# Kernel optimization log

Hardware: AMD Instinct MI355X
Metric: run time of the kernel (lower is better)

Reference implementation:

```python
import jax, jax.numpy as jnp
import numpy as np

N = 50000
E = 800000
F_IN = 128
HID = 32
HEADS = 4
SLOPE = 0.2


def setup_inputs() -> dict:
    key = jax.random.key(0)
    ks = jax.random.split(key, 12)
    x = jax.random.normal(ks[0], (N, F_IN), dtype=jnp.float32)
    edge_index = jax.random.randint(ks[1], (2, E), 0, N, dtype=jnp.int64)
    edge_attr = jax.random.normal(ks[2], (E, 4), dtype=jnp.float32)
    s1 = 1.0 / np.sqrt(F_IN)
    s2 = 1.0 / np.sqrt(HID)
    W1 = jax.random.normal(ks[3], (F_IN, HEADS * HID), dtype=jnp.float32) * s1
    a_src1 = jax.random.normal(ks[4], (HEADS, HID), dtype=jnp.float32) * s2
    a_dst1 = jax.random.normal(ks[5], (HEADS, HID), dtype=jnp.float32) * s2
    b1 = jnp.zeros((HID,), dtype=jnp.float32)
    W2 = jax.random.normal(ks[6], (HID, 1), dtype=jnp.float32) * s2
    a_src2 = jax.random.normal(ks[7], (1, 1), dtype=jnp.float32)
    a_dst2 = jax.random.normal(ks[8], (1, 1), dtype=jnp.float32)
    b2 = jnp.zeros((1,), dtype=jnp.float32)
    return {"input_tensor": x, "edge_index": edge_index, "edge_attr": edge_attr,
            "W1": W1, "a_src1": a_src1, "a_dst1": a_dst1, "b1": b1,
            "W2": W2, "a_src2": a_src2, "a_dst2": a_dst2, "b2": b2}


def _gat_conv(x, src, dst, W, a_src, a_dst, b, heads, out_ch):
    n = x.shape[0]
    h = (x @ W).reshape(n, heads, out_ch)          # [N, H, C]
    alpha_src = jnp.sum(h * a_src, axis=-1)        # [N, H]
    alpha_dst = jnp.sum(h * a_dst, axis=-1)        # [N, H]
    e = alpha_src[src] + alpha_dst[dst]            # [E, H]
    e = jax.nn.leaky_relu(e, negative_slope=SLOPE)
    # segment softmax over edges grouped by destination node
    e_max = jax.ops.segment_max(e, dst, num_segments=n)
    e = jnp.exp(e - e_max[dst])
    denom = jax.ops.segment_sum(e, dst, num_segments=n)
    alpha = e / denom[dst]                         # [E, H]
    msg = h[src] * alpha[..., None]                # [E, H, C]
    out = jax.ops.segment_sum(msg, dst, num_segments=n)  # [N, H, C]
    return out.mean(axis=1) + b                    # concat=False -> mean over heads


def reference(input_tensor, edge_index, edge_attr, W1, a_src1, a_dst1, b1, W2, a_src2, a_dst2, b2):
    # PyG GATConv adds self-loops by default; edge_attr unused (edge_dim=None)
    loops = jnp.arange(N, dtype=edge_index.dtype)
    src = jnp.concatenate([edge_index[0], loops])
    dst = jnp.concatenate([edge_index[1], loops])
    x = _gat_conv(input_tensor, src, dst, W1, a_src1, a_dst1, b1, HEADS, HID)
    x = jax.nn.elu(x)
    x = _gat_conv(x, src, dst, W2, a_src2, a_dst2, b2, 1, 1)
    return x
```

## Files before the change

kernel.cpp:

```cpp
#include <hip/hip_runtime.h>
#include <hip/hip_fp16.h>
#include <math.h>
#include <stdint.h>

static constexpr int kN     = 50000;
static constexpr int kFIn   = 128;
static constexpr int kHeads = 4;
static constexpr int kScanB = 256;
static constexpr int kScanNB = (kN + kScanB - 1) / kScanB;

typedef _Float16 half8v  __attribute__((ext_vector_type(8)));
typedef float    floatx4 __attribute__((ext_vector_type(4)));

__device__ __forceinline__ float lrelu(float x) { return x > 0.f ? x : 0.2f * x; }

__device__ __forceinline__ float pack2h(float a, float b) {
    const __half2 h = __floats2half2_rn(a, b);
    return __uint_as_float(__builtin_bit_cast(uint32_t, h));
}

__global__ void k_init(int* __restrict__ p, int n) {
    int i = blockIdx.x * blockDim.x + threadIdx.x;
    if (i < n) p[i] = 0;
}

__global__ __launch_bounds__(256)
void k_gemm1(const float* __restrict__ x, const float* __restrict__ W1,
             __half* __restrict__ h1h, int nPass, int grid) {
    __shared__ __align__(16) float whf[128 * 16 * 4];
    __shared__ __align__(16) float xsf[32 * 16 * 4];
    const int t = threadIdx.x;
    const int l = t & 63;
    const int g = t >> 6;
    for (int idx = t; idx < 2048; idx += 256) {
        const int c = idx >> 7, col = idx & 127;
        float4 st;
        st.x = pack2h(W1[(8 * c + 0) * 128 + col], W1[(8 * c + 1) * 128 + col]);
        st.y = pack2h(W1[(8 * c + 2) * 128 + col], W1[(8 * c + 3) * 128 + col]);
        st.z = pack2h(W1[(8 * c + 4) * 128 + col], W1[(8 * c + 5) * 128 + col]);
        st.w = pack2h(W1[(8 * c + 6) * 128 + col], W1[(8 * c + 7) * 128 + col]);
        const int gran = col * 16 + ((c + col) & 15);
        *reinterpret_cast<float4*>(&whf[gran * 4]) = st;
    }
    __syncthreads();

    const int rt  = g & 1;
    const int ctB = (g >> 1) * 4;
    const int lm  = l & 15;
    const int lk  = l >> 4;

    for (int pass = blockIdx.x; pass < nPass; pass += grid) {
        const int nodeBase = pass * 32;
        for (int q = t; q < 512; q += 256) {
            const int nn = q >> 4, ck = q & 15;
            int n = nodeBase + nn; if (n >= kN) n = kN - 1;
            const float4 xa = *reinterpret_cast<const float4*>(&x[(size_t)n * 128 + ck * 8]);
            const float4 xb = *reinterpret_cast<const float4*>(&x[(size_t)n * 128 + ck * 8 + 4]);
            float4 st;
            st.x = pack2h(xa.x, xa.y);
            st.y = pack2h(xa.z, xa.w);
            st.z = pack2h(xb.x, xb.y);
            st.w = pack2h(xb.z, xb.w);
            const int gran = nn * 16 + ((ck + nn) & 15);
            *reinterpret_cast<float4*>(&xsf[gran * 4]) = st;
        }
        __syncthreads();

        floatx4 acc0 = {0.f, 0.f, 0.f, 0.f};
        floatx4 acc1 = {0.f, 0.f, 0.f, 0.f};
        floatx4 acc2 = {0.f, 0.f, 0.f, 0.f};
        floatx4 acc3 = {0.f, 0.f, 0.f, 0.f};
        const int node = rt * 16 + lm;
        const int ch0  = ctB * 16 + lm;
#pragma unroll
        for (int kk = 0; kk < 4; ++kk) {
            const int ck = lk + 4 * kk;
            const half8v af = *reinterpret_cast<const half8v*>(
                &xsf[(node * 16 + ((ck + node) & 15)) * 4]);
            const half8v b0 = *reinterpret_cast<const half8v*>(
                &whf[((ch0 +  0) * 16 + ((ck + ch0 +  0) & 15)) * 4]);
            const half8v b1 = *reinterpret_cast<const half8v*>(
                &whf[((ch0 + 16) * 16 + ((ck + ch0 + 16) & 15)) * 4]);
            const half8v b2 = *reinterpret_cast<const half8v*>(
                &whf[((ch0 + 32) * 16 + ((ck + ch0 + 32) & 15)) * 4]);
            const half8v b3 = *reinterpret_cast<const half8v*>(
                &whf[((ch0 + 48) * 16 + ((ck + ch0 + 48) & 15)) * 4]);
            acc0 = __builtin_amdgcn_mfma_f32_16x16x32_f16(af, b0, acc0, 0, 0, 0);
            acc1 = __builtin_amdgcn_mfma_f32_16x16x32_f16(af, b1, acc1, 0, 0, 0);
            acc2 = __builtin_amdgcn_mfma_f32_16x16x32_f16(af, b2, acc2, 0, 0, 0);
            acc3 = __builtin_amdgcn_mfma_f32_16x16x32_f16(af, b3, acc3, 0, 0, 0);
        }
        const int nrow0 = nodeBase + rt * 16 + lk * 4;
#pragma unroll
        for (int r = 0; r < 4; ++r) {
            const int n = nrow0 + r;
            if (n < kN) {
                h1h[(size_t)n * 128 + ch0     ] = __float2half(acc0[r]);
                h1h[(size_t)n * 128 + ch0 + 16] = __float2half(acc1[r]);
                h1h[(size_t)n * 128 + ch0 + 32] = __float2half(acc2[r]);
                h1h[(size_t)n * 128 + ch0 + 48] = __float2half(acc3[r]);
            }
        }
        __syncthreads();
    }
}

__global__ __launch_bounds__(256)
void k_logits(const __half* __restrict__ h1h,
              const float* __restrict__ a_src1, const float* __restrict__ a_dst1,
              float* __restrict__ asrc, float* __restrict__ adst) {
    const int n = blockIdx.x * 4 + (threadIdx.x >> 6);
    if (n >= kN) return;
    const int j = threadIdx.x & 63;
    const float2 f = __half22float2(*(const __half2*)&h1h[(size_t)n * 128 + 2 * j]);
    float ps = f.x * a_src1[2 * j] + f.y * a_src1[2 * j + 1];
    float pd = f.x * a_dst1[2 * j] + f.y * a_dst1[2 * j + 1];
#pragma unroll
    for (int off = 8; off >= 1; off >>= 1) {
        ps += __shfl_xor(ps, off, 64);
        pd += __shfl_xor(pd, off, 64);
    }
    if ((j & 15) == 0) {
        asrc[n * 4 + (j >> 4)] = ps;
        adst[n * 4 + (j >> 4)] = pd;
    }
}

__global__ void k_hist(const int* __restrict__ ei, int E, int* __restrict__ deg,
                       int* __restrict__ rank) {
    int i = blockIdx.x * blockDim.x + threadIdx.x;
    int total = E + kN;
    if (i >= total) return;
    int d = (i < E) ? ei[E + i] : (i - E);
    rank[i] = atomicAdd(&deg[d], 1);
}

__global__ void k_scan_a(const int* __restrict__ deg, int* __restrict__ loc, int* __restrict__ bsum) {
    __shared__ int tmp[kScanB];
    int t = threadIdx.x;
    int i = blockIdx.x * kScanB + t;
    int v = (i < kN) ? deg[i] : 0;
    tmp[t] = v;
    __syncthreads();
    for (int off = 1; off < kScanB; off <<= 1) {
        int add = (t >= off) ? tmp[t - off] : 0;
        __syncthreads();
        tmp[t] += add;
        __syncthreads();
    }
    if (i < kN) loc[i] = tmp[t] - v;
    if (t == kScanB - 1) bsum[blockIdx.x] = tmp[t];
}

__global__ void k_scan_b(int* __restrict__ bsum) {
    __shared__ int tmp[256];
    int t = threadIdx.x;
    int v = (t < kScanNB) ? bsum[t] : 0;
    tmp[t] = v;
    __syncthreads();
    for (int off = 1; off < 256; off <<= 1) {
        int add = (t >= off) ? tmp[t - off] : 0;
        __syncthreads();
        tmp[t] += add;
        __syncthreads();
    }
    if (t < kScanNB) bsum[t] = tmp[t] - v;
}

__global__ void k_scan_c(const int* __restrict__ loc, const int* __restrict__ bsum,
                         int* __restrict__ rowptr, int E2) {
    int i = blockIdx.x * kScanB + threadIdx.x;
    if (i < kN) rowptr[i] = loc[i] + bsum[blockIdx.x];
    if (i == 0) rowptr[kN] = E2;
}

__global__ void k_scatter(const int* __restrict__ ei, int E,
                          const int* __restrict__ rowptr, const int* __restrict__ rank,
                          int* __restrict__ es) {
    int i = blockIdx.x * blockDim.x + threadIdx.x;
    int total = E + kN;
    if (i >= total) return;
    int s, d;
    if (i < E) { s = ei[i]; d = ei[E + i]; } else { s = d = i - E; }
    es[rowptr[d] + rank[i]] = s;
}

__global__ __launch_bounds__(256)
void k_wgt(const int* __restrict__ rowptr, const int* __restrict__ es,
           const float* __restrict__ asrc, const float* __restrict__ adst,
           __half* __restrict__ alphaH) {
    const int n = blockIdx.x * 16 + (threadIdx.x >> 4);
    if (n >= kN) return;
    const int l = threadIdx.x & 15;
    const int beg = rowptr[n], end = rowptr[n + 1];
    const float ad0 = adst[n * 4 + 0], ad1 = adst[n * 4 + 1];
    const float ad2 = adst[n * 4 + 2], ad3 = adst[n * 4 + 3];
    float t0 = 0.f, t1 = 0.f, t2 = 0.f, t3 = 0.f;
    for (int p = beg + l; p < end; p += 16) {
        const int s = es[p];
        t0 += expf(lrelu(asrc[s * 4 + 0] + ad0));
        t1 += expf(lrelu(asrc[s * 4 + 1] + ad1));
        t2 += expf(lrelu(asrc[s * 4 + 2] + ad2));
        t3 += expf(lrelu(asrc[s * 4 + 3] + ad3));
    }
#pragma unroll
    for (int off = 8; off >= 1; off >>= 1) {
        t0 += __shfl_xor(t0, off, 64);
        t1 += __shfl_xor(t1, off, 64);
        t2 += __shfl_xor(t2, off, 64);
        t3 += __shfl_xor(t3, off, 64);
    }
    const float r0 = 1.f / t0, r1 = 1.f / t1, r2 = 1.f / t2, r3 = 1.f / t3;
    for (int p = beg + l; p < end; p += 16) {
        const int s = es[p];
        const float w0 = expf(lrelu(asrc[s * 4 + 0] + ad0)) * r0;
        const float w1 = expf(lrelu(asrc[s * 4 + 1] + ad1)) * r1;
        const float w2 = expf(lrelu(asrc[s * 4 + 2] + ad2)) * r2;
        const float w3 = expf(lrelu(asrc[s * 4 + 3] + ad3)) * r3;
        float2 st;
        st.x = pack2h(w0, w1);
        st.y = pack2h(w2, w3);
        *reinterpret_cast<float2*>(&alphaH[(size_t)p * 4]) = st;
    }
}

__global__ __launch_bounds__(256)
void k_agg1(const int* __restrict__ rowptr, const int* __restrict__ es,
            const __half* __restrict__ alphaH,
            const __half* __restrict__ h1h, const float* __restrict__ b1,
            const float* __restrict__ W2, float* __restrict__ h2) {
    const int n = blockIdx.x * 4 + (threadIdx.x >> 6);
    if (n >= kN) return;
    const int j  = threadIdx.x & 63;
    const int hh = j >> 4;
    const int beg = rowptr[n], end = rowptr[n + 1];
    const __half2* h12 = (const __half2*)h1h;
    __half2 accA = __floats2half2_rn(0.f, 0.f);
    __half2 accB = __floats2half2_rn(0.f, 0.f);
    int p = beg;
    for (; p + 4 <= end; p += 4) {
        const int s0 = es[p],     s1 = es[p + 1];
        const int s2 = es[p + 2], s3 = es[p + 3];
        const __half a0 = alphaH[(size_t)(p + 0) * 4 + hh];
        const __half a1 = alphaH[(size_t)(p + 1) * 4 + hh];
        const __half a2 = alphaH[(size_t)(p + 2) * 4 + hh];
        const __half a3 = alphaH[(size_t)(p + 3) * 4 + hh];
        const __half2 v0 = h12[(size_t)s0 * 64 + j];
        const __half2 v1 = h12[(size_t)s1 * 64 + j];
        const __half2 v2 = h12[(size_t)s2 * 64 + j];
        const __half2 v3 = h12[(size_t)s3 * 64 + j];
        accA = __hfma2(__half2half2(a0), v0, accA);
        accB = __hfma2(__half2half2(a1), v1, accB);
        accA = __hfma2(__half2half2(a2), v2, accA);
        accB = __hfma2(__half2half2(a3), v3, accB);
    }
    for (; p < end; ++p) {
        const int s0 = es[p];
        const __half a0 = alphaH[(size_t)p * 4 + hh];
        accA = __hfma2(__half2half2(a0), h12[(size_t)s0 * 64 + j], accA);
    }
    const float2 fa = __half22float2(accA);
    const float2 fb = __half22float2(accB);
    float vx = fa.x + fb.x;
    float vy = fa.y + fb.y;
    vx += __shfl_xor(vx, 32, 64); vy += __shfl_xor(vy, 32, 64);
    vx += __shfl_xor(vx, 16, 64); vy += __shfl_xor(vy, 16, 64);
    const int m = j & 15;
    float u0 = 0.25f * vx + b1[2 * m];
    float u1 = 0.25f * vy + b1[2 * m + 1];
    u0 = u0 > 0.f ? u0 : expf(u0) - 1.f;
    u1 = u1 > 0.f ? u1 : expf(u1) - 1.f;
    float tsum = u0 * W2[2 * m] + u1 * W2[2 * m + 1];
    tsum += __shfl_xor(tsum, 8, 64);
    tsum += __shfl_xor(tsum, 4, 64);
    tsum += __shfl_xor(tsum, 2, 64);
    tsum += __shfl_xor(tsum, 1, 64);
    if (j == 0) h2[n] = tsum;
}

__global__ __launch_bounds__(256)
void k_agg2(const int* __restrict__ rowptr, const int* __restrict__ es,
            const float* __restrict__ h2,
            const float* __restrict__ a_s2, const float* __restrict__ a_d2,
            const float* __restrict__ b2, float* __restrict__ out) {
    const int n = blockIdx.x * 16 + (threadIdx.x >> 4);
    if (n >= kN) return;
    const int l = threadIdx.x & 15;
    const float as = a_s2[0], ad = a_d2[0];
    const int beg = rowptr[n], end = rowptr[n + 1];
    const float hd = h2[n] * ad;
    float sw = 0.f, swh = 0.f;
    for (int p = beg + l; p < end; p += 16) {
        float hs = h2[es[p]];
        float w = expf(lrelu(hs * as + hd));
        sw += w;
        swh += w * hs;
    }
#pragma unroll
    for (int off = 8; off >= 1; off >>= 1) {
        sw  += __shfl_xor(sw, off, 64);
        swh += __shfl_xor(swh, off, 64);
    }
    if (l == 0) out[n] = swh / sw + b2[0];
}

extern "C" void kernel_launch(void* const* d_in, const int* in_sizes, int n_in,
                              void* d_out, int out_size, void* d_ws, size_t ws_size,
                              hipStream_t stream) {
    const float* x      = (const float*)d_in[0];
    const int*   ei     = (const int*)d_in[1];
    const float* W1     = (const float*)d_in[3];
    const float* a_src1 = (const float*)d_in[4];
    const float* a_dst1 = (const float*)d_in[5];
    const float* b1     = (const float*)d_in[6];
    const float* W2     = (const float*)d_in[7];
    const float* a_src2 = (const float*)d_in[8];
    const float* a_dst2 = (const float*)d_in[9];
    const float* b2     = (const float*)d_in[10];
    float* out = (float*)d_out;

    const int E  = in_sizes[1] / 2;
    const int E2 = E + kN;

    float*  ws    = (float*)d_ws;
    float*  asrc  = ws;
    float*  adst  = ws + 200000;
    float*  h2    = ws + 400000;
    __half* h1h   = (__half*)(ws + 450000);
    __half* alphaH= (__half*)(ws + 3650000);
    int*    ibase = (int*)(ws + 5350000);
    int*    es     = ibase;
    int*    deg    = ibase + 850000;
    int*    rank   = ibase + 900000;
    int*    loc    = ibase + 1750000;
    int*    rowptr = ibase + 1800000;
    int*    bsum   = ibase + 1850016;

    k_init<<<(kN + 255) / 256, 256, 0, stream>>>(deg, kN);

    k_hist<<<(E2 + 255) / 256, 256, 0, stream>>>(ei, E, deg, rank);
    k_scan_a<<<kScanNB, kScanB, 0, stream>>>(deg, loc, bsum);
    k_scan_b<<<1, 256, 0, stream>>>(bsum);
    k_scan_c<<<kScanNB, kScanB, 0, stream>>>(loc, bsum, rowptr, E2);

    {
        const int nPass = (kN + 31) / 32;
        const int grid  = 782;
        k_gemm1<<<grid, 256, 0, stream>>>(x, W1, h1h, nPass, grid);
    }

    k_logits<<<(kN + 3) / 4, 256, 0, stream>>>(h1h, a_src1, a_dst1, asrc, adst);

    k_scatter<<<(E2 + 255) / 256, 256, 0, stream>>>(ei, E, rowptr, rank, es);

    k_wgt<<<(kN + 15) / 16, 256, 0, stream>>>(rowptr, es, asrc, adst, alphaH);

    k_agg1<<<(kN + 3) / 4, 256, 0, stream>>>(rowptr, es, alphaH, h1h, b1, W2, h2);

    k_agg2<<<(kN + 15) / 16, 256, 0, stream>>>(rowptr, es, h2, a_src2, a_dst2, b2, out);
}
```

Measured before the change: 147.5 us.

## Split layer-1 aggregation per head into partial sums plus a finish kernel

Result: slower. 172.3 us (+16.9%).

```diff
diff --git a/kernel.cpp b/kernel.cpp
--- a/kernel.cpp
+++ b/kernel.cpp
@@ -225,49 +225,53 @@
 }
 
 __global__ __launch_bounds__(256)
-void k_agg1(const int* __restrict__ rowptr, const int* __restrict__ es,
-            const __half* __restrict__ alphaH,
-            const __half* __restrict__ h1h, const float* __restrict__ b1,
-            const float* __restrict__ W2, float* __restrict__ h2) {
-    const int n = blockIdx.x * 4 + (threadIdx.x >> 6);
-    if (n >= kN) return;
-    const int j  = threadIdx.x & 63;
-    const int hh = j >> 4;
+void k_agg1h(const int* __restrict__ rowptr, const int* __restrict__ es,
+             const __half* __restrict__ alphaH, const __half* __restrict__ h1h,
+             __half2* __restrict__ part) {
+    const int b    = blockIdx.x;
+    const int head = (b & 7) >> 1;
+    const int rank = (b >> 3) * 2 + (b & 1);
+    const int g    = threadIdx.x >> 6;
+    const int l    = threadIdx.x & 63;
+    const int sub  = l >> 4;
+    const int m    = l & 15;
+    const int n    = rank * 16 + g * 4 + sub;
+    if (n >= kN) return;
     const int beg = rowptr[n], end = rowptr[n + 1];
     const __half2* h12 = (const __half2*)h1h;
+    const int chOff = head * 16 + m;
     __half2 accA = __floats2half2_rn(0.f, 0.f);
     __half2 accB = __floats2half2_rn(0.f, 0.f);
     int p = beg;
-    for (; p + 4 <= end; p += 4) {
-        const int s0 = es[p],     s1 = es[p + 1];
-        const int s2 = es[p + 2], s3 = es[p + 3];
-        const __half a0 = alphaH[(size_t)(p + 0) * 4 + hh];
-        const __half a1 = alphaH[(size_t)(p + 1) * 4 + hh];
-        const __half a2 = alphaH[(size_t)(p + 2) * 4 + hh];
-        const __half a3 = alphaH[(size_t)(p + 3) * 4 + hh];
-        const __half2 v0 = h12[(size_t)s0 * 64 + j];
-        const __half2 v1 = h12[(size_t)s1 * 64 + j];
-        const __half2 v2 = h12[(size_t)s2 * 64 + j];
-        const __half2 v3 = h12[(size_t)s3 * 64 + j];
-        accA = __hfma2(__half2half2(a0), v0, accA);
-        accB = __hfma2(__half2half2(a1), v1, accB);
-        accA = __hfma2(__half2half2(a2), v2, accA);
-        accB = __hfma2(__half2half2(a3), v3, accB);
-    }
-    for (; p < end; ++p) {
+    for (; p + 2 <= end; p += 2) {
+        const int s0 = es[p], s1 = es[p + 1];
+        const __half a0 = alphaH[(size_t)p * 4 + head];
+        const __half a1 = alphaH[(size_t)(p + 1) * 4 + head];
+        accA = __hfma2(__half2half2(a0), h12[(size_t)s0 * 64 + chOff], accA);
+        accB = __hfma2(__half2half2(a1), h12[(size_t)s1 * 64 + chOff], accB);
+    }
+    if (p < end) {
         const int s0 = es[p];
-        const __half a0 = alphaH[(size_t)p * 4 + hh];
-        accA = __hfma2(__half2half2(a0), h12[(size_t)s0 * 64 + j], accA);
-    }
-    const float2 fa = __half22float2(accA);
-    const float2 fb = __half22float2(accB);
-    float vx = fa.x + fb.x;
-    float vy = fa.y + fb.y;
-    vx += __shfl_xor(vx, 32, 64); vy += __shfl_xor(vy, 32, 64);
-    vx += __shfl_xor(vx, 16, 64); vy += __shfl_xor(vy, 16, 64);
-    const int m = j & 15;
-    float u0 = 0.25f * vx + b1[2 * m];
-    float u1 = 0.25f * vy + b1[2 * m + 1];
+        const __half a0 = alphaH[(size_t)p * 4 + head];
+        accA = __hfma2(__half2half2(a0), h12[(size_t)s0 * 64 + chOff], accA);
+    }
+    part[((size_t)head * kN + n) * 16 + m] = __hadd2(accA, accB);
+}
+
+__global__ __launch_bounds__(256)
+void k_finish(const __half2* __restrict__ part, const float* __restrict__ b1,
+              const float* __restrict__ W2, float* __restrict__ h2) {
+    const int n = blockIdx.x * 16 + (threadIdx.x >> 4);
+    if (n >= kN) return;
+    const int m = threadIdx.x & 15;
+    float sx = 0.f, sy = 0.f;
+#pragma unroll
+    for (int h = 0; h < kHeads; ++h) {
+        const float2 v = __half22float2(part[((size_t)h * kN + n) * 16 + m]);
+        sx += v.x; sy += v.y;
+    }
+    float u0 = 0.25f * sx + b1[2 * m];
+    float u1 = 0.25f * sy + b1[2 * m + 1];
     u0 = u0 > 0.f ? u0 : expf(u0) - 1.f;
     u1 = u1 > 0.f ? u1 : expf(u1) - 1.f;
     float tsum = u0 * W2[2 * m] + u1 * W2[2 * m + 1];
@@ -275,7 +279,7 @@
     tsum += __shfl_xor(tsum, 4, 64);
     tsum += __shfl_xor(tsum, 2, 64);
     tsum += __shfl_xor(tsum, 1, 64);
-    if (j == 0) h2[n] = tsum;
+    if (m == 0) h2[n] = tsum;
 }
 
 __global__ __launch_bounds__(256)
@@ -322,19 +326,20 @@
     const int E  = in_sizes[1] / 2;
     const int E2 = E + kN;
 
-    float*  ws    = (float*)d_ws;
-    float*  asrc  = ws;
-    float*  adst  = ws + 200000;
-    float*  h2    = ws + 400000;
-    __half* h1h   = (__half*)(ws + 450000);
-    __half* alphaH= (__half*)(ws + 3650000);
-    int*    ibase = (int*)(ws + 5350000);
-    int*    es     = ibase;
-    int*    deg    = ibase + 850000;
-    int*    rank   = ibase + 900000;
-    int*    loc    = ibase + 1750000;
-    int*    rowptr = ibase + 1800000;
-    int*    bsum   = ibase + 1850016;
+    float*   ws     = (float*)d_ws;
+    float*   asrc   = ws;
+    float*   adst   = ws + 200000;
+    float*   h2     = ws + 400000;
+    __half*  h1h    = (__half*)(ws + 450000);
+    __half*  alphaH = (__half*)(ws + 3650000);
+    __half2* part   = (__half2*)(ws + 5350000);
+    int*     ibase  = (int*)(ws + 8550000);
+    int*     es     = ibase;
+    int*     deg    = ibase + 850000;
+    int*     rank   = ibase + 900000;
+    int*     loc    = ibase + 1750000;
+    int*     rowptr = ibase + 1800000;
+    int*     bsum   = ibase + 1850016;
 
     k_init<<<(kN + 255) / 256, 256, 0, stream>>>(deg, kN);
 
@@ -355,7 +360,12 @@
 
     k_wgt<<<(kN + 15) / 16, 256, 0, stream>>>(rowptr, es, asrc, adst, alphaH);
 
-    k_agg1<<<(kN + 3) / 4, 256, 0, stream>>>(rowptr, es, alphaH, h1h, b1, W2, h2);
+    {
+        const int grid = 8 * 1563;
+        k_agg1h<<<grid, 256, 0, stream>>>(rowptr, es, alphaH, h1h, part);
+    }
+
+    k_finish<<<(kN + 15) / 16, 256, 0, stream>>>(part, b1, W2, h2);
 
     k_agg2<<<(kN + 15) / 16, 256, 0, stream>>>(rowptr, es, h2, a_src2, a_dst2, b2, out);
 }
```

## Merge degree histogram into GEMM1 launch via block-index split

Applied to the files above, without the earlier changes.

Measured after the change: 137.6 us. 6.7% less time.

```diff
diff --git a/kernel.cpp b/kernel.cpp
--- a/kernel.cpp
+++ b/kernel.cpp
@@ -8,6 +8,7 @@
 static constexpr int kHeads = 4;
 static constexpr int kScanB = 256;
 static constexpr int kScanNB = (kN + kScanB - 1) / kScanB;
+static constexpr int kGemmGrid = 782;
 
 typedef _Float16 half8v  __attribute__((ext_vector_type(8)));
 typedef float    floatx4 __attribute__((ext_vector_type(4)));
@@ -25,10 +26,23 @@
 }
 
 __global__ __launch_bounds__(256)
-void k_gemm1(const float* __restrict__ x, const float* __restrict__ W1,
-             __half* __restrict__ h1h, int nPass, int grid) {
+void k_gemm1_hist(const float* __restrict__ x, const float* __restrict__ W1,
+                  __half* __restrict__ h1h, int nPass,
+                  const int* __restrict__ ei, int E,
+                  int* __restrict__ deg, int* __restrict__ rank) {
     __shared__ __align__(16) float whf[128 * 16 * 4];
     __shared__ __align__(16) float xsf[32 * 16 * 4];
+
+    if (blockIdx.x >= kGemmGrid) {
+        const int i = (blockIdx.x - kGemmGrid) * 256 + threadIdx.x;
+        const int total = E + kN;
+        if (i < total) {
+            const int d = (i < E) ? ei[E + i] : (i - E);
+            rank[i] = atomicAdd(&deg[d], 1);
+        }
+        return;
+    }
+
     const int t = threadIdx.x;
     const int l = t & 63;
     const int g = t >> 6;
@@ -49,7 +63,7 @@
     const int lm  = l & 15;
     const int lk  = l >> 4;
 
-    for (int pass = blockIdx.x; pass < nPass; pass += grid) {
+    for (int pass = blockIdx.x; pass < nPass; pass += kGemmGrid) {
         const int nodeBase = pass * 32;
         for (int q = t; q < 512; q += 256) {
             const int nn = q >> 4, ck = q & 15;
@@ -124,15 +138,6 @@
         asrc[n * 4 + (j >> 4)] = ps;
         adst[n * 4 + (j >> 4)] = pd;
     }
-}
-
-__global__ void k_hist(const int* __restrict__ ei, int E, int* __restrict__ deg,
-                       int* __restrict__ rank) {
-    int i = blockIdx.x * blockDim.x + threadIdx.x;
-    int total = E + kN;
-    if (i >= total) return;
-    int d = (i < E) ? ei[E + i] : (i - E);
-    rank[i] = atomicAdd(&deg[d], 1);
 }
 
 __global__ void k_scan_a(const int* __restrict__ deg, int* __restrict__ loc, int* __restrict__ bsum) {
@@ -322,35 +327,35 @@
     const int E  = in_sizes[1] / 2;
     const int E2 = E + kN;
 
-    float*  ws    = (float*)d_ws;
-    float*  asrc  = ws;
-    float*  adst  = ws + 200000;
-    float*  h2    = ws + 400000;
-    __half* h1h   = (__half*)(ws + 450000);
-    __half* alphaH= (__half*)(ws + 3650000);
-    int*    ibase = (int*)(ws + 5350000);
-    int*    es     = ibase;
-    int*    deg    = ibase + 850000;
-    int*    rank   = ibase + 900000;
-    int*    loc    = ibase + 1750000;
-    int*    rowptr = ibase + 1800000;
-    int*    bsum   = ibase + 1850016;
+    float*   ws     = (float*)d_ws;
+    float*   asrc   = ws;
+    float*   adst   = ws + 200000;
+    float*   h2     = ws + 400000;
+    __half*  h1h    = (__half*)(ws + 450000);
+    __half*  alphaH = (__half*)(ws + 3650000);
+    int*     ibase  = (int*)(ws + 5350000);
+    int*     es     = ibase;
+    int*     deg    = ibase + 850000;
+    int*     rank   = ibase + 900000;
+    int*     loc    = ibase + 1750000;
+    int*     rowptr = ibase + 1800000;
+    int*     bsum   = ibase + 1850016;
 
     k_init<<<(kN + 255) / 256, 256, 0, stream>>>(deg, kN);
 
-    k_hist<<<(E2 + 255) / 256, 256, 0, stream>>>(ei, E, deg, rank);
+    {
+        const int nPass      = (kN + 31) / 32;
+        const int histBlocks = (E2 + 255) / 256;
+        k_gemm1_hist<<<kGemmGrid + histBlocks, 256, 0, stream>>>(
+            x, W1, h1h, nPass, ei, E, deg, rank);
+    }
+
+    k_logits<<<(kN + 3) / 4, 256, 0, stream>>>(h1h, a_src1, a_dst1, asrc, adst);
+
     k_scan_a<<<kScanNB, kScanB, 0, stream>>>(deg, loc, bsum);
     k_scan_b<<<1, 256, 0, stream>>>(bsum);
     k_scan_c<<<kScanNB, kScanB, 0, stream>>>(loc, bsum, rowptr, E2);
 
-    {
-        const int nPass = (kN + 31) / 32;
-        const int grid  = 782;
-        k_gemm1<<<grid, 256, 0, stream>>>(x, W1, h1h, nPass, grid);
-    }
-
-    k_logits<<<(kN + 3) / 4, 256, 0, stream>>>(h1h, a_src1, a_dst1, asrc, adst);
-
     k_scatter<<<(E2 + 255) / 256, 256, 0, stream>>>(ei, E, rowptr, rank, es);
 
     k_wgt<<<(kN + 15) / 16, 256, 0, stream>>>(rowptr, es, asrc, adst, alphaH);
```
